# Kernel tuning notes

Measured on AMD Instinct MI355X. Metric: run time of the kernel, lower is better.

## Reference

```python
import jax, jax.numpy as jnp
import numpy as np

B = 16384
ED = 32          # embed_dim
NF = 16          # num_filters
KS = [1, 3, 5, 7, 9]
LENS = {"pep": 12, "a1": 7, "a2": 8, "a3": 22, "b1": 6, "b2": 7, "b3": 23}


def setup_inputs() -> dict:
    key = jax.random.key(0)
    keys = jax.random.split(key, 32)
    ki = iter(keys)
    inp = {}
    for name, L in LENS.items():
        inp[name] = jax.random.normal(next(ki), (B, ED, L), dtype=jnp.float32)
    # conv weights: one stack of 7 convs per kernel size; w{k}: [7, NF, ED, k], bias c{k}: [7, NF]
    for k in KS:
        fan_in = ED * k
        bound = 1.0 / np.sqrt(fan_in)
        inp[f"w{k}"] = jax.random.uniform(next(ki), (7, NF, ED, k), jnp.float32, -bound, bound)
        inp[f"c{k}"] = jax.random.uniform(next(ki), (7, NF), jnp.float32, -bound, bound)
    dbound = 1.0 / np.sqrt(NF * 35)
    inp["dw"] = jax.random.uniform(next(ki), (NF * 35, 1), jnp.float32, -dbound, dbound)
    inp["db"] = jax.random.uniform(next(ki), (1,), jnp.float32, -dbound, dbound)
    return inp


def _branch(x, w, b):
    # x: [B, ED, L], w: [NF, ED, k], b: [NF] -> [B, NF] (conv 'same' + relu + global max)
    y = jax.lax.conv_general_dilated(x, w, window_strides=(1,), padding="SAME",
                                     dimension_numbers=("NCH", "OIH", "NCH"))
    y = jax.nn.relu(y + b[None, :, None])
    return jnp.max(y, axis=2)


def reference(pep, a1, a2, a3, b1, b2, b3, w1, w3, w5, w7, w9, c1, c3, c5, c7, c9, dw, db):
    xs = [pep, a1, a2, a3, b1, b2, b3]
    ws = {1: w1, 3: w3, 5: w5, 7: w7, 9: w9}
    cs = {1: c1, 3: c3, 5: c5, 7: c7, 9: c9}
    feats = []
    for i, x in enumerate(xs):  # fixed 7 inputs
        for k in KS:            # fixed 5 kernel sizes
            feats.append(_branch(x, ws[k][i], cs[k][i]))
    feat = jnp.concatenate(feats, axis=1)        # [B, 35*NF]
    out = jax.nn.sigmoid(feat @ dw + db)         # [B, 1]
    return jnp.squeeze(out, axis=-1)             # [B]
```

## Files before the change

kernel.cpp:

```cpp
#include <hip/hip_runtime.h>
#include <cmath>

namespace {

using bf16x8 = __attribute__((ext_vector_type(8))) short;
using f32x4  = __attribute__((ext_vector_type(4))) float;

constexpr int NT = 192;
constexpr int NS = 16;
constexpr int LPAD = 31;
constexpr int TILE_BYTES = NS * LPAD * 32 * 2;

__device__ __forceinline__ short f2bf(float f) {
  unsigned u = __float_as_uint(f);
  unsigned r = (u + 0x7FFFu + ((u >> 16) & 1u)) >> 16;
  return (short)r;
}

__device__ __forceinline__ int gidx(int s, int q, int cq) {
  return (s * 31 + q) * 4 + ((cq ^ ((s >> 1) + (q >> 1))) & 3);
}

__device__ __forceinline__ bf16x8 ldcol(const char* smem, int s, int cq, int q) {
  return *(const bf16x8*)(smem + (gidx(s, q, cq) << 4));
}

template<int K1, int K2>
__device__ __forceinline__ void run_role(
    const char* __restrict__ smem, int s, int cq, int f,
    const float* __restrict__ wk1, const float* __restrict__ ck1,
    const float* __restrict__ wk2, const float* __restrict__ ck2,
    const float* __restrict__ dw, int i, int L, f32x4& dvec)
{
  constexpr int KK1 = (K1 - 1) / 2;
  constexpr int KK2 = (K2 > 0) ? (K2 - 1) / 2 : 0;

  bf16x8 wf1[K1];
  #pragma unroll
  for (int t = 0; t < K1; ++t) {
    const float* wp = wk1 + (size_t)((i * 16 + f) * 32 + cq * 8) * K1 + t;
    bf16x8 v;
    #pragma unroll
    for (int j = 0; j < 8; ++j) v[j] = f2bf(wp[(size_t)j * K1]);
    wf1[t] = v;
  }
  bf16x8 wf2[(K2 > 0) ? K2 : 1];
  if constexpr (K2 > 0) {
    #pragma unroll
    for (int t = 0; t < K2; ++t) {
      const float* wp = wk2 + (size_t)((i * 16 + f) * 32 + cq * 8) * K2 + t;
      bf16x8 v;
      #pragma unroll
      for (int j = 0; j < 8; ++j) v[j] = f2bf(wp[(size_t)j * K2]);
      wf2[t] = v;
    }
  }

  const float b1 = ck1[i * 16 + f];
  float b2 = 0.f;
  if constexpr (K2 > 0) b2 = ck2[i * 16 + f];

  f32x4 mx1 = {0.f, 0.f, 0.f, 0.f};
  f32x4 mx2 = {0.f, 0.f, 0.f, 0.f};

  bf16x8 af[K1];
  #pragma unroll
  for (int j = 0; j < K1; ++j) af[j] = ldcol(smem, s, cq, 4 - KK1 + j);

  auto body = [&](int p, int pi) {
    f32x4 aa = {b1, b1, b1, b1};
    f32x4 ab = {0.f, 0.f, 0.f, 0.f};
    #pragma unroll
    for (int t = 0; t < K1; ++t) {
      if (t & 1)
        ab = __builtin_amdgcn_mfma_f32_16x16x32_bf16(af[(pi + t) % K1], wf1[t], ab, 0, 0, 0);
      else
        aa = __builtin_amdgcn_mfma_f32_16x16x32_bf16(af[(pi + t) % K1], wf1[t], aa, 0, 0, 0);
    }
    if constexpr (K2 > 0) {
      f32x4 ac = {b2, b2, b2, b2};
      #pragma unroll
      for (int t = 0; t < K2; ++t)
        ac = __builtin_amdgcn_mfma_f32_16x16x32_bf16(af[(pi + (KK1 - KK2) + t) % K1], wf2[t], ac, 0, 0, 0);
      #pragma unroll
      for (int r = 0; r < 4; ++r) mx2[r] = fmaxf(mx2[r], ac[r]);
    }
    #pragma unroll
    for (int r = 0; r < 4; ++r) mx1[r] = fmaxf(mx1[r], aa[r] + ab[r]);
    if (p + pi + 1 < L)
      af[pi] = ldcol(smem, s, cq, p + pi + 5 + KK1);
  };

  int p = 0;
  for (; p + K1 <= L; p += K1) {
    #pragma unroll
    for (int pi = 0; pi < K1; ++pi) body(p, pi);
  }
  #pragma unroll
  for (int pi = 0; pi < K1 - 1; ++pi)
    if (p + pi < L) body(p, pi);

  {
    const float dv1 = dw[(i * 5 + KK1) * 16 + f];
    #pragma unroll
    for (int r = 0; r < 4; ++r) dvec[r] = fmaf(mx1[r], dv1, dvec[r]);
  }
  if constexpr (K2 > 0) {
    const float dv2 = dw[(i * 5 + KK2) * 16 + f];
    #pragma unroll
    for (int r = 0; r < 4; ++r) dvec[r] = fmaf(mx2[r], dv2, dvec[r]);
  }
}

__global__ __launch_bounds__(NT, 3) void nettcr_mfma(
    const float* __restrict__ x0, const float* __restrict__ x1,
    const float* __restrict__ x2, const float* __restrict__ x3,
    const float* __restrict__ x4, const float* __restrict__ x5,
    const float* __restrict__ x6,
    const float* __restrict__ w1, const float* __restrict__ c1,
    const float* __restrict__ w3, const float* __restrict__ c3,
    const float* __restrict__ w5, const float* __restrict__ c5,
    const float* __restrict__ w7, const float* __restrict__ c7,
    const float* __restrict__ w9, const float* __restrict__ c9,
    const float* __restrict__ dw, const float* __restrict__ db,
    float* __restrict__ out)
{
  __shared__ __align__(16) char smem[TILE_BYTES];
  const int tid  = threadIdx.x;
  const int lane = tid & 63;
  const int wid  = tid >> 6;
  const int s    = lane & 15;
  const int cq   = lane >> 4;
  const int f    = lane & 15;
  const int b0   = blockIdx.x * NS;

  f32x4 dvec = {0.f, 0.f, 0.f, 0.f};

  for (int i = 0; i < 7; ++i) {
    const float* xi; int L;
    switch (i) {
      case 0: xi = x0; L = 12; break;
      case 1: xi = x1; L = 7;  break;
      case 2: xi = x2; L = 8;  break;
      case 3: xi = x3; L = 22; break;
      case 4: xi = x4; L = 6;  break;
      case 5: xi = x5; L = 7;  break;
      default: xi = x6; L = 23; break;
    }
    __syncthreads();
    for (int e = tid; e < 64 * L; e += NT) {
      const int l  = e % L;
      const int rr = e / L;
      const int cg = rr & 3;
      const int ss = rr >> 2;
      const float* src = xi + ((size_t)(b0 + ss) * 32 + cg * 8) * L + l;
      bf16x8 pk;
      #pragma unroll
      for (int j = 0; j < 8; ++j) pk[j] = f2bf(src[(size_t)j * L]);
      *(bf16x8*)(smem + (gidx(ss, l + 4, cg) << 4)) = pk;
    }
    for (int e = tid; e < 512; e += NT) {
      const int q8 = e & 7;
      const int q  = (q8 < 4) ? q8 : (L + q8);
      const int cg = (e >> 3) & 3;
      const int ss = e >> 5;
      bf16x8 z = {0, 0, 0, 0, 0, 0, 0, 0};
      *(bf16x8*)(smem + (gidx(ss, q, cg) << 4)) = z;
    }
    __syncthreads();

    if (wid == 0)
      run_role<9, 0>(smem, s, cq, f, w9, c9, nullptr, nullptr, dw, i, L, dvec);
    else if (wid == 1)
      run_role<7, 1>(smem, s, cq, f, w7, c7, w1, c1, dw, i, L, dvec);
    else
      run_role<5, 3>(smem, s, cq, f, w5, c5, w3, c3, dw, i, L, dvec);
  }

  __syncthreads();
  float* red = (float*)smem;
  *(f32x4*)&red[(wid * 64 + lane) * 4] = dvec;
  __syncthreads();
  if (tid < 16) {
    float sum = db[0];
    const int g4 = tid >> 2, r = tid & 3;
    for (int w = 0; w < 3; ++w)
      #pragma unroll
      for (int f2 = 0; f2 < 16; ++f2)
        sum += red[(w * 64 + g4 * 16 + f2) * 4 + r];
    out[b0 + tid] = 1.0f / (1.0f + expf(-sum));
  }
}

}

extern "C" void kernel_launch(void* const* d_in, const int* in_sizes, int n_in,
                              void* d_out, int out_size, void* d_ws, size_t ws_size,
                              hipStream_t stream) {
  (void)d_ws; (void)ws_size; (void)out_size;
  const float* xs[7];
  for (int i = 0; i < 7; ++i) xs[i] = (const float*)d_in[i];

  const float* wptr[5] = {nullptr, nullptr, nullptr, nullptr, nullptr};
  const float* cptr[5] = {nullptr, nullptr, nullptr, nullptr, nullptr};
  const float* dw = nullptr;
  const float* db = nullptr;
  int c_seen = 0;
  for (int idx = 7; idx < n_in; ++idx) {
    const int sz = in_sizes[idx];
    const float* p = (const float*)d_in[idx];
    if (sz == 1) { db = p; }
    else if (sz == 16 * 35) { dw = p; }
    else if (sz == 7 * 16) { cptr[c_seen++] = p; }
    else {
      const int k = sz / (7 * 16 * 32);
      wptr[(k - 1) / 2] = p;
    }
  }

  float* out = (float*)d_out;
  const int B = 16384;
  dim3 grid(B / NS), block(NT);
  hipLaunchKernelGGL(nettcr_mfma, grid, block, 0, stream,
                     xs[0], xs[1], xs[2], xs[3], xs[4], xs[5], xs[6],
                     wptr[0], cptr[0], wptr[1], cptr[1], wptr[2], cptr[2],
                     wptr[3], cptr[3], wptr[4], cptr[4], dw, db, out);
}
```

Before: 98.56 us.

## Split inputs across two blocks per sample tile and prepack bf16 weights

Pre-converts all conv weights once into packed bf16x8 granules in workspace, so each wave loads weights with single vector loads instead of eight strided fp32 loads plus conversions per input. Doubles the grid so each 16-sample tile is handled by two blocks, one taking inputs 0,3,5 and the other 1,2,4,6, to balance the sequence lengths. Partial logits go to workspace and a third kernel sums them and applies the sigmoid. It also uses three accumulator chains for the K=7 and K=9 convolutions to shorten MFMA dependency chains. This costs two extra launches and a workspace round trip.

```diff
diff --git a/kernel.cpp b/kernel.cpp
--- a/kernel.cpp
+++ b/kernel.cpp
@@ -8,13 +8,16 @@
 
 constexpr int NT = 192;
 constexpr int NS = 16;
-constexpr int LPAD = 31;
-constexpr int TILE_BYTES = NS * LPAD * 32 * 2;
+constexpr int TILE_BYTES = NS * 31 * 32 * 2;
+constexpr int B = 16384;
+
+constexpr int WOFF1 = 0, WOFF3 = 448, WOFF5 = 1792, WOFF7 = 4032, WOFF9 = 7168;
+constexpr int WGRANULES = 11200;
+constexpr int PART_OFF_FLOATS = WGRANULES * 4;
 
 __device__ __forceinline__ short f2bf(float f) {
   unsigned u = __float_as_uint(f);
-  unsigned r = (u + 0x7FFFu + ((u >> 16) & 1u)) >> 16;
-  return (short)r;
+  return (short)((u + 0x7FFFu + ((u >> 16) & 1u)) >> 16);
 }
 
 __device__ __forceinline__ int gidx(int s, int q, int cq) {
@@ -28,32 +31,23 @@
 template<int K1, int K2>
 __device__ __forceinline__ void run_role(
     const char* __restrict__ smem, int s, int cq, int f,
-    const float* __restrict__ wk1, const float* __restrict__ ck1,
-    const float* __restrict__ wk2, const float* __restrict__ ck2,
+    const bf16x8* __restrict__ wg1, const float* __restrict__ ck1,
+    const bf16x8* __restrict__ wg2, const float* __restrict__ ck2,
     const float* __restrict__ dw, int i, int L, f32x4& dvec)
 {
   constexpr int KK1 = (K1 - 1) / 2;
   constexpr int KK2 = (K2 > 0) ? (K2 - 1) / 2 : 0;
+  constexpr int NCH = (K1 >= 7) ? 3 : 2;
 
   bf16x8 wf1[K1];
   #pragma unroll
-  for (int t = 0; t < K1; ++t) {
-    const float* wp = wk1 + (size_t)((i * 16 + f) * 32 + cq * 8) * K1 + t;
-    bf16x8 v;
-    #pragma unroll
-    for (int j = 0; j < 8; ++j) v[j] = f2bf(wp[(size_t)j * K1]);
-    wf1[t] = v;
-  }
+  for (int t = 0; t < K1; ++t)
+    wf1[t] = wg1[((i * 16 + f) * 4 + cq) * K1 + t];
   bf16x8 wf2[(K2 > 0) ? K2 : 1];
   if constexpr (K2 > 0) {
     #pragma unroll
-    for (int t = 0; t < K2; ++t) {
-      const float* wp = wk2 + (size_t)((i * 16 + f) * 32 + cq * 8) * K2 + t;
-      bf16x8 v;
-      #pragma unroll
-      for (int j = 0; j < 8; ++j) v[j] = f2bf(wp[(size_t)j * K2]);
-      wf2[t] = v;
-    }
+    for (int t = 0; t < K2; ++t)
+      wf2[t] = wg2[((i * 16 + f) * 4 + cq) * K2 + t];
   }
 
   const float b1 = ck1[i * 16 + f];
@@ -68,25 +62,33 @@
   for (int j = 0; j < K1; ++j) af[j] = ldcol(smem, s, cq, 4 - KK1 + j);
 
   auto body = [&](int p, int pi) {
-    f32x4 aa = {b1, b1, b1, b1};
-    f32x4 ab = {0.f, 0.f, 0.f, 0.f};
+    f32x4 ca = {b1, b1, b1, b1};
+    f32x4 cb = {0.f, 0.f, 0.f, 0.f};
+    f32x4 cc = {0.f, 0.f, 0.f, 0.f};
     #pragma unroll
     for (int t = 0; t < K1; ++t) {
-      if (t & 1)
-        ab = __builtin_amdgcn_mfma_f32_16x16x32_bf16(af[(pi + t) % K1], wf1[t], ab, 0, 0, 0);
+      const int m = t % NCH;
+      if (m == 0)
+        ca = __builtin_amdgcn_mfma_f32_16x16x32_bf16(af[(pi + t) % K1], wf1[t], ca, 0, 0, 0);
+      else if (m == 1)
+        cb = __builtin_amdgcn_mfma_f32_16x16x32_bf16(af[(pi + t) % K1], wf1[t], cb, 0, 0, 0);
       else
-        aa = __builtin_amdgcn_mfma_f32_16x16x32_bf16(af[(pi + t) % K1], wf1[t], aa, 0, 0, 0);
+        cc = __builtin_amdgcn_mfma_f32_16x16x32_bf16(af[(pi + t) % K1], wf1[t], cc, 0, 0, 0);
     }
     if constexpr (K2 > 0) {
-      f32x4 ac = {b2, b2, b2, b2};
+      f32x4 cd = {b2, b2, b2, b2};
       #pragma unroll
       for (int t = 0; t < K2; ++t)
-        ac = __builtin_amdgcn_mfma_f32_16x16x32_bf16(af[(pi + (KK1 - KK2) + t) % K1], wf2[t], ac, 0, 0, 0);
-      #pragma unroll
-      for (int r = 0; r < 4; ++r) mx2[r] = fmaxf(mx2[r], ac[r]);
-    }
-    #pragma unroll
-    for (int r = 0; r < 4; ++r) mx1[r] = fmaxf(mx1[r], aa[r] + ab[r]);
+        cd = __builtin_amdgcn_mfma_f32_16x16x32_bf16(af[(pi + (KK1 - KK2) + t) % K1], wf2[t], cd, 0, 0, 0);
+      #pragma unroll
+      for (int r = 0; r < 4; ++r) mx2[r] = fmaxf(mx2[r], cd[r]);
+    }
+    #pragma unroll
+    for (int r = 0; r < 4; ++r) {
+      float tot = ca[r] + cb[r];
+      if constexpr (NCH == 3) tot += cc[r];
+      mx1[r] = fmaxf(mx1[r], tot);
+    }
     if (p + pi + 1 < L)
       af[pi] = ldcol(smem, s, cq, p + pi + 5 + KK1);
   };
@@ -110,6 +112,30 @@
     #pragma unroll
     for (int r = 0; r < 4; ++r) dvec[r] = fmaf(mx2[r], dv2, dvec[r]);
   }
+}
+
+__global__ void prep_weights(const float* __restrict__ w1, const float* __restrict__ w3,
+                             const float* __restrict__ w5, const float* __restrict__ w7,
+                             const float* __restrict__ w9, bf16x8* __restrict__ out)
+{
+  const int g = blockIdx.x * blockDim.x + threadIdx.x;
+  if (g >= WGRANULES) return;
+  int k, base; const float* w;
+  if (g < WOFF3)      { k = 1; base = WOFF1; w = w1; }
+  else if (g < WOFF5) { k = 3; base = WOFF3; w = w3; }
+  else if (g < WOFF7) { k = 5; base = WOFF5; w = w5; }
+  else if (g < WOFF9) { k = 7; base = WOFF7; w = w7; }
+  else                { k = 9; base = WOFF9; w = w9; }
+  const int r  = g - base;
+  const int t  = r % k;
+  const int u  = r / k;
+  const int fi = u >> 2;
+  const int cg = u & 3;
+  bf16x8 v;
+  #pragma unroll
+  for (int j = 0; j < 8; ++j)
+    v[j] = f2bf(w[(size_t)(fi * 32 + cg * 8 + j) * k + t]);
+  out[g] = v;
 }
 
 __global__ __launch_bounds__(NT, 3) void nettcr_mfma(
@@ -117,35 +143,41 @@
     const float* __restrict__ x2, const float* __restrict__ x3,
     const float* __restrict__ x4, const float* __restrict__ x5,
     const float* __restrict__ x6,
-    const float* __restrict__ w1, const float* __restrict__ c1,
-    const float* __restrict__ w3, const float* __restrict__ c3,
-    const float* __restrict__ w5, const float* __restrict__ c5,
-    const float* __restrict__ w7, const float* __restrict__ c7,
-    const float* __restrict__ w9, const float* __restrict__ c9,
-    const float* __restrict__ dw, const float* __restrict__ db,
-    float* __restrict__ out)
+    const float* __restrict__ c1, const float* __restrict__ c3,
+    const float* __restrict__ c5, const float* __restrict__ c7,
+    const float* __restrict__ c9,
+    const float* __restrict__ dw,
+    const bf16x8* __restrict__ wg,
+    float* __restrict__ part)
 {
   __shared__ __align__(16) char smem[TILE_BYTES];
   const int tid  = threadIdx.x;
   const int lane = tid & 63;
   const int wid  = tid >> 6;
+  const int h    = blockIdx.x & 1;
+  const int b0   = (blockIdx.x >> 1) * NS;
   const int s    = lane & 15;
   const int cq   = lane >> 4;
   const int f    = lane & 15;
-  const int b0   = blockIdx.x * NS;
 
   f32x4 dvec = {0.f, 0.f, 0.f, 0.f};
 
-  for (int i = 0; i < 7; ++i) {
-    const float* xi; int L;
-    switch (i) {
-      case 0: xi = x0; L = 12; break;
-      case 1: xi = x1; L = 7;  break;
-      case 2: xi = x2; L = 8;  break;
-      case 3: xi = x3; L = 22; break;
-      case 4: xi = x4; L = 6;  break;
-      case 5: xi = x5; L = 7;  break;
-      default: xi = x6; L = 23; break;
+  const int nin = h ? 4 : 3;
+  for (int j = 0; j < nin; ++j) {
+    const float* xi; int i, L;
+    if (h == 0) {
+      switch (j) {
+        case 0:  i = 0; xi = x0; L = 12; break;
+        case 1:  i = 3; xi = x3; L = 22; break;
+        default: i = 5; xi = x5; L = 7;  break;
+      }
+    } else {
+      switch (j) {
+        case 0:  i = 1; xi = x1; L = 7;  break;
+        case 1:  i = 2; xi = x2; L = 8;  break;
+        case 2:  i = 4; xi = x4; L = 6;  break;
+        default: i = 6; xi = x6; L = 23; break;
+      }
     }
     __syncthreads();
     for (int e = tid; e < 64 * L; e += NT) {
@@ -156,7 +188,7 @@
       const float* src = xi + ((size_t)(b0 + ss) * 32 + cg * 8) * L + l;
       bf16x8 pk;
       #pragma unroll
-      for (int j = 0; j < 8; ++j) pk[j] = f2bf(src[(size_t)j * L]);
+      for (int jj = 0; jj < 8; ++jj) pk[jj] = f2bf(src[(size_t)jj * L]);
       *(bf16x8*)(smem + (gidx(ss, l + 4, cg) << 4)) = pk;
     }
     for (int e = tid; e < 512; e += NT) {
@@ -170,11 +202,11 @@
     __syncthreads();
 
     if (wid == 0)
-      run_role<9, 0>(smem, s, cq, f, w9, c9, nullptr, nullptr, dw, i, L, dvec);
+      run_role<9, 0>(smem, s, cq, f, (const bf16x8*)wg + WOFF9, c9, nullptr, nullptr, dw, i, L, dvec);
     else if (wid == 1)
-      run_role<7, 1>(smem, s, cq, f, w7, c7, w1, c1, dw, i, L, dvec);
+      run_role<7, 1>(smem, s, cq, f, (const bf16x8*)wg + WOFF7, c7, (const bf16x8*)wg + WOFF1, c1, dw, i, L, dvec);
     else
-      run_role<5, 3>(smem, s, cq, f, w5, c5, w3, c3, dw, i, L, dvec);
+      run_role<5, 3>(smem, s, cq, f, (const bf16x8*)wg + WOFF5, c5, (const bf16x8*)wg + WOFF3, c3, dw, i, L, dvec);
   }
 
   __syncthreads();
@@ -182,13 +214,24 @@
   *(f32x4*)&red[(wid * 64 + lane) * 4] = dvec;
   __syncthreads();
   if (tid < 16) {
-    float sum = db[0];
+    float sum = 0.f;
     const int g4 = tid >> 2, r = tid & 3;
     for (int w = 0; w < 3; ++w)
       #pragma unroll
       for (int f2 = 0; f2 < 16; ++f2)
         sum += red[(w * 64 + g4 * 16 + f2) * 4 + r];
-    out[b0 + tid] = 1.0f / (1.0f + expf(-sum));
+    part[h * B + b0 + tid] = sum;
+  }
+}
+
+__global__ void combine_sigmoid(const float* __restrict__ part,
+                                const float* __restrict__ db,
+                                float* __restrict__ out)
+{
+  const int i = blockIdx.x * blockDim.x + threadIdx.x;
+  if (i < B) {
+    const float sum = part[i] + part[B + i] + db[0];
+    out[i] = 1.0f / (1.0f + expf(-sum));
   }
 }
 
@@ -197,7 +240,7 @@
 extern "C" void kernel_launch(void* const* d_in, const int* in_sizes, int n_in,
                               void* d_out, int out_size, void* d_ws, size_t ws_size,
                               hipStream_t stream) {
-  (void)d_ws; (void)ws_size; (void)out_size;
+  (void)ws_size; (void)out_size;
   const float* xs[7];
   for (int i = 0; i < 7; ++i) xs[i] = (const float*)d_in[i];
 
@@ -218,11 +261,18 @@
     }
   }
 
-  float* out = (float*)d_out;
-  const int B = 16384;
-  dim3 grid(B / NS), block(NT);
+  bf16x8* wg   = (bf16x8*)d_ws;
+  float*  part = (float*)d_ws + PART_OFF_FLOATS;
+
+  hipLaunchKernelGGL(prep_weights, dim3((WGRANULES + 255) / 256), dim3(256), 0, stream,
+                     wptr[0], wptr[1], wptr[2], wptr[3], wptr[4], wg);
+
+  dim3 grid(2 * (B / NS)), block(NT);
   hipLaunchKernelGGL(nettcr_mfma, grid, block, 0, stream,
                      xs[0], xs[1], xs[2], xs[3], xs[4], xs[5], xs[6],
-                     wptr[0], cptr[0], wptr[1], cptr[1], wptr[2], cptr[2],
-                     wptr[3], cptr[3], wptr[4], cptr[4], dw, db, out);
-}
+                     cptr[0], cptr[1], cptr[2], cptr[3], cptr[4],
+                     dw, wg, part);
+
+  hipLaunchKernelGGL(combine_sigmoid, dim3((B + 255) / 256), dim3(256), 0, stream,
+                     part, db, (float*)d_out);
+}
```

Result: slower. 215.1 us (+118.2%).
